# Kernel tuning notes

Measured on AMD Instinct MI355X. Metric: run time of the kernel, lower is better.

## Reference

```python
import jax, jax.numpy as jnp
import numpy as np

B, S, NH, D_IN = 64, 512, 4, 256   # batch, seq_len, rnn n_head, input_dim
H = 256                            # hidden_dim == attention activation_dim
AH = 256                           # attention_hidden_dim (attn out_dim)
OUT = 3                            # output_dim (sentiment classes)


def setup_inputs() -> dict:
    key = jax.random.key(0)
    ks = jax.random.split(key, 9)
    def p(k, shape, scale=0.05):
        return jax.random.normal(k, shape, dtype=jnp.float32) * scale
    return dict(
        x=jax.random.normal(ks[0], (B, S, NH, D_IN), dtype=jnp.float32),
        Wk=p(ks[1], (D_IN, H)), bk=jnp.zeros((H,), jnp.float32),
        Wq=p(ks[2], (H, H)),    bq=jnp.zeros((H,), jnp.float32),
        w_mlp=p(ks[3], (2 * H,)),
        Wproj=p(ks[4], (H, AH)), bproj=jnp.zeros((AH,), jnp.float32),
        W1=p(ks[5], (D_IN + AH, H)), b1=jnp.zeros((H,), jnp.float32),
        W2=p(ks[6], (H, H)),    b2=jnp.zeros((H,), jnp.float32),
        Wo=p(ks[7], (NH * H, OUT)), bo=jnp.zeros((OUT,), jnp.float32),
    )


def _cell(x_t, hidden, params):
    Wk, bk, Wq, bq, w_mlp, Wproj, bproj, W1, b1, W2, b2, Wo, bo = params
    kx = x_t @ Wk + bk           # [B, NH, H]  keys from step input
    qx = hidden @ Wq + bq        # [B, NH, H]  queries from hidden state
    w1, w2 = w_mlp[:H], w_mlp[H:]
    # MLP score: s[b,i,j] = tanh(cat(kx[b,j], qx[b,i]) . w) = tanh(kx[b,j].w1 + qx[b,i].w2)
    score = jnp.tanh((qx @ w2)[:, :, None] + (kx @ w1)[:, None, :])  # [B, NH, NH]
    score = jax.nn.softmax(score, axis=-1)
    attn = jnp.einsum('bij,bjh->bih', score, kx) @ Wproj + bproj     # [B, NH, AH]
    concat = jnp.concatenate([x_t, attn], axis=-1)                   # [B, NH, D_IN+AH]
    hidden_new = jax.nn.relu(concat @ W1 + b1) @ W2 + b2             # [B, NH, H]
    logits = hidden_new.reshape(B, NH * H) @ Wo + bo                 # [B, OUT]
    out = jax.nn.log_softmax(logits, axis=-1)
    return out, hidden_new


def reference(x, Wk, bk, Wq, bq, w_mlp, Wproj, bproj, W1, b1, W2, b2, Wo, bo):
    params = (Wk, bk, Wq, bq, w_mlp, Wproj, bproj, W1, b1, W2, b2, Wo, bo)
    h0 = jnp.zeros((B, NH, H), x.dtype)
    xs = jnp.swapaxes(x, 0, 1)  # [S, B, NH, D_IN] for scan over time
    def step(h, x_t):
        out, h_new = _cell(x_t, h, params)
        return h_new, out
    h_final, outs = jax.lax.scan(step, h0, xs)
    # return_sequence=False: last-step log-softmax output and final hidden
    return outs[-1], h_final
```

## Files before the change

kernel.cpp:

```cpp
#include <hip/hip_runtime.h>
#include <hip/hip_bf16.h>
#include <math.h>

#define BB   64
#define SS   512
#define NHH  4
#define DD   256
#define HH   256
#define LDH  264

typedef __attribute__((ext_vector_type(8))) short  short8;
typedef __attribute__((ext_vector_type(4))) float  floatx4;


__device__ __forceinline__ unsigned short f2b(float f) {
  __hip_bfloat16 h = __float2bfloat16(f);
  return __builtin_bit_cast(unsigned short, h);
}
__device__ __forceinline__ float b2f(unsigned short u) {
  unsigned v = (unsigned)u << 16;
  return __builtin_bit_cast(float, v);
}

__global__ __launch_bounds__(256) void init1_kernel(
    const float* __restrict__ Wk, const float* __restrict__ Wproj,
    const float* __restrict__ W1, const float* __restrict__ Wq,
    const float* __restrict__ bq, const float* __restrict__ w_mlp,
    const float* __restrict__ W2, const float* __restrict__ b2,
    const float* __restrict__ bk,
    float* __restrict__ ws, unsigned short* __restrict__ wpack)
{
  __shared__ float vsh[256];
  __shared__ float red[256];
  int tid = threadIdx.x;
  int b = blockIdx.x;

  if (b == 0) {
    const float* w2 = w_mlp + HH;
    {
      float a = 0.f;
      const float4* Wq4 = (const float4*)(Wq + tid * 256);
      const float4* w24 = (const float4*)w2;
      for (int k = 0; k < 64; ++k) {
        float4 wv = Wq4[k], xv = w24[k];
        a = fmaf(wv.x, xv.x, fmaf(wv.y, xv.y, fmaf(wv.z, xv.z, fmaf(wv.w, xv.w, a))));
      }
      vsh[tid] = a;
    }
    __syncthreads();
    {
      float a2 = 0.f;
      const float4* W24 = (const float4*)(W2 + tid * 256);
      const float4* v4  = (const float4*)vsh;
      for (int k = 0; k < 64; ++k) {
        float4 wv = W24[k], xv = v4[k];
        a2 = fmaf(wv.x, xv.x, fmaf(wv.y, xv.y, fmaf(wv.z, xv.z, fmaf(wv.w, xv.w, a2))));
      }
      ws[tid] = a2;
    }
    red[tid] = bq[tid] * w_mlp[HH + tid];
    __syncthreads();
    for (int s = 128; s; s >>= 1) { if (tid < s) red[tid] += red[tid + s]; __syncthreads(); }
    float c = red[0];
    __syncthreads();
    ws[768 + tid] = c;
    red[tid] = b2[tid] * vsh[tid];
    __syncthreads();
    for (int s = 128; s; s >>= 1) { if (tid < s) red[tid] += red[tid + s]; __syncthreads(); }
    if (tid == 0) ws[512] = red[0] + c;
    __syncthreads();
    red[tid] = bk[tid] * w_mlp[tid];
    __syncthreads();
    for (int s = 128; s; s >>= 1) { if (tid < s) red[tid] += red[tid + s]; __syncthreads(); }
    if (tid == 0) ws[513] = red[0];
    return;
  }

  if (b <= 256) {
    int idx = (b - 1) * 256 + tid;
    int j    = idx & 7;
    int lane = (idx >> 3) & 63;
    int ks   = (idx >> 9) & 7;
    int pan  = idx >> 12;
    int k = ks * 32 + ((lane >> 4) << 3) + j;
    int n = pan * 16 + (lane & 15);
    wpack[idx] = f2b(W1[k * 256 + n]);
    return;
  }

  {
    int r = b - 257;
    const float* w1b = W1 + 256 * 256;
    float acc = 0.f;
    for (int k = 0; k < 256; ++k)
      acc = fmaf(Wproj[r * 256 + k], w1b[k * 256 + tid], acc);
    ws[132096 + r * 256 + tid] = acc;
  }
}

__global__ __launch_bounds__(256) void init2_kernel(
    const float* __restrict__ Wk, const float* __restrict__ W1,
    const float* __restrict__ bproj, const float* __restrict__ bk,
    const float* __restrict__ w_mlp,
    float* __restrict__ ws, unsigned short* __restrict__ wpack)
{
  __shared__ float red[256];
  int tid = threadIdx.x;
  int b = blockIdx.x;
  const float* Wc = ws + 132096;

  if (b < 256) {
    int r = b;
    float acc = 0.f;
    for (int k = 0; k < 256; ++k)
      acc = fmaf(Wk[r * 256 + k], Wc[k * 256 + tid], acc);
    int n = tid;
    int pan = n >> 4, ks = r >> 5, j = r & 7;
    int lane = ((r >> 3) & 3) * 16 + (n & 15);
    wpack[65536 + pan * 4096 + ks * 512 + lane * 8 + j] = f2b(acc);
    red[tid] = Wk[r * 256 + tid] * w_mlp[tid];
    __syncthreads();
    for (int s = 128; s; s >>= 1) { if (tid < s) red[tid] += red[tid + s]; __syncthreads(); }
    if (tid == 0) ws[197632 + r] = red[0];
    return;
  }

  {
    const float* w1b = W1 + 256 * 256;
    float a3 = 0.f;
    for (int k = 0; k < 256; ++k)
      a3 = fmaf(bproj[k], w1b[k * 256 + tid], a3);
    for (int k = 0; k < 256; ++k)
      a3 = fmaf(bk[k], Wc[k * 256 + tid], a3);
    ws[256 + tid] = a3;
  }
}

__device__ __forceinline__ void mfma_gemm4(
    const unsigned short* A_lds, const short8* __restrict__ Bp,
    const float* __restrict__ bias, floatx4 acc[4][4], int l, int w)
{
  int col = l & 15, quad = l >> 4;
#pragma unroll
  for (int pp = 0; pp < 4; ++pp) {
    float bv = bias ? bias[(w * 4 + pp) * 16 + col] : 0.f;
#pragma unroll
    for (int mf = 0; mf < 4; ++mf)
      acc[mf][pp] = (floatx4){bv, bv, bv, bv};
  }
  const short8* Bb = Bp + (size_t)(w * 4) * 512 + l;
  short8 bb[3][4];
  short8 aa[2][4];
#pragma unroll
  for (int pp = 0; pp < 4; ++pp) bb[0][pp] = Bb[pp * 512];
#pragma unroll
  for (int pp = 0; pp < 4; ++pp) bb[1][pp] = Bb[pp * 512 + 64];
#pragma unroll
  for (int mf = 0; mf < 4; ++mf)
    aa[0][mf] = *(const short8*)(A_lds + (mf * 16 + col) * LDH + quad * 8);
#pragma unroll
  for (int kb = 0; kb < 8; ++kb) {
    if (kb + 2 < 8) {
#pragma unroll
      for (int pp = 0; pp < 4; ++pp)
        bb[(kb + 2) % 3][pp] = Bb[pp * 512 + (kb + 2) * 64];
    }
    if (kb + 1 < 8) {
#pragma unroll
      for (int mf = 0; mf < 4; ++mf)
        aa[(kb + 1) & 1][mf] =
            *(const short8*)(A_lds + (mf * 16 + col) * LDH + (kb + 1) * 32 + quad * 8);
    }
#pragma unroll
    for (int mf = 0; mf < 4; ++mf)
#pragma unroll
      for (int pp = 0; pp < 4; ++pp)
        acc[mf][pp] = __builtin_amdgcn_mfma_f32_16x16x32_bf16(
            aa[kb & 1][mf], bb[kb % 3][pp], acc[mf][pp], 0, 0, 0);
  }
}

__device__ __forceinline__ void acc_to_global(
    unsigned short* __restrict__ dst, const floatx4 acc[4][4],
    int l, int w, int b, int tt)
{
  int col = l & 15, quad = l >> 4;
#pragma unroll
  for (int mf = 0; mf < 4; ++mf)
#pragma unroll
    for (int r = 0; r < 4; ++r) {
      int m2 = mf * 16 + quad * 4 + r;
      size_t base = (((size_t)(tt * 16 + (m2 >> 2)) * 64 + b) * 4 + (m2 & 3)) * 256;
#pragma unroll
      for (int pp = 0; pp < 4; ++pp)
        dst[base + (w * 4 + pp) * 16 + col] = f2b(acc[mf][pp][r]);
    }
}

__device__ void precompute_block(
    int px, const float* __restrict__ x, const unsigned short* __restrict__ wpack,
    const float* __restrict__ b1, const float* __restrict__ ws,
    float* __restrict__ kw_c, unsigned short* __restrict__ xw1_c,
    unsigned short* __restrict__ kpw_c, int t0, char* smem)
{
  float* kwbuf = (float*)smem;
  unsigned short* XS = (unsigned short*)(smem + 2048);

  int b  = px & 63;
  int tt = px >> 6;
  int tid = threadIdx.x;
  int l = tid & 63, w = tid >> 6;

  const float4* xsrc = (const float4*)(x + (size_t)(b * SS + t0 + tt * 16) * NHH * DD);
#pragma unroll
  for (int i = 0; i < 16; ++i) {
    int f4 = i * 256 + tid;
    int r = f4 >> 6, c4 = f4 & 63;
    float4 v = xsrc[f4];
    ushort4 h;
    h.x = f2b(v.x); h.y = f2b(v.y); h.z = f2b(v.z); h.w = f2b(v.w);
    *(ushort4*)&XS[r * LDH + c4 * 4] = h;
  }
  __syncthreads();

  const short8* wpA = (const short8*)(wpack);
  const short8* wpD = (const short8*)(wpack + 65536);

  {
    const float* wkw = ws + 197632;
    float part = 0.f;
    const unsigned short* trow = XS + l * LDH + w * 64;
#pragma unroll
    for (int j8 = 0; j8 < 8; ++j8) {
      short8 tv = *(const short8*)(trow + j8 * 8);
#pragma unroll
      for (int j = 0; j < 8; ++j)
        part = fmaf(b2f((unsigned short)tv[j]), wkw[w * 64 + j8 * 8 + j], part);
    }
    kwbuf[l * 4 + w] = part;
  }

  floatx4 acc[4][4];

  mfma_gemm4(XS, wpA, b1, acc, l, w);
  acc_to_global(xw1_c, acc, l, w, b, tt);

  mfma_gemm4(XS, wpD, nullptr, acc, l, w);
  acc_to_global(kpw_c, acc, l, w, b, tt);

  __syncthreads();
  if (tid < 64) {
    float s = kwbuf[tid * 4] + kwbuf[tid * 4 + 1] + kwbuf[tid * 4 + 2] + kwbuf[tid * 4 + 3]
            + ws[513];
    kw_c[((size_t)(tt * 16 + (tid >> 2)) * 64 + b) * 4 + (tid & 3)] = s;
  }
}

__device__ __forceinline__ float wave_reduce_sum(float x) {
#define DPPSTEP(ctrl, rmask)                                                   \
  {                                                                            \
    int _s = __builtin_amdgcn_update_dpp(0, __builtin_bit_cast(int, x),        \
                                         (ctrl), (rmask), 0xf, true);          \
    x += __builtin_bit_cast(float, _s);                                        \
  }
  DPPSTEP(0x111, 0xf)
  DPPSTEP(0x112, 0xf)
  DPPSTEP(0x114, 0xf)
  DPPSTEP(0x118, 0xf)
  DPPSTEP(0x142, 0xa)
  DPPSTEP(0x143, 0xc)
#undef DPPSTEP
  return __builtin_bit_cast(float, __builtin_amdgcn_readlane(__builtin_bit_cast(int, x), 63));
}

__device__ __forceinline__ float tanh_fast(float y) {
  float ex = __expf(2.f * y);
  return 1.f - 2.f * __builtin_amdgcn_rcpf(ex + 1.f);
}

__device__ void seq_block(
    const unsigned short* __restrict__ xw1_c, const unsigned short* __restrict__ kpw_c,
    const float* __restrict__ kw_c, float* __restrict__ ws,
    float* __restrict__ relu_u, int t0, int n)
{
  int b = blockIdx.x;
  int tid = threadIdx.x;
  int i = tid >> 6, l = tid & 63;

  float4 v2v = ((const float4*)ws)[l];
  float4 cbv = ((const float4*)(ws + 256))[l];
  float c2 = ws[512];
  float qw = ws[768 + b * 4 + i];

  const ushort4* xw = (const ushort4*)xw1_c;
  const ushort4* kp = (const ushort4*)kpw_c;

  struct Slot { ushort4 x, k0, k1, k2, k3; float4 kw; };

  auto load = [&](Slot& s, int tc) {
    size_t rb_ = (size_t)(tc * 64 + b) * 4;
    s.x  = xw[(rb_ + i) * 64 + l];
    s.k0 = kp[(rb_ + 0) * 64 + l];
    s.k1 = kp[(rb_ + 1) * 64 + l];
    s.k2 = kp[(rb_ + 2) * 64 + l];
    s.k3 = kp[(rb_ + 3) * 64 + l];
    s.kw = *(const float4*)&kw_c[rb_];
  };

  auto step = [&](Slot& s, int t) {
    float e0 = tanh_fast(qw + s.kw.x);
    float e1 = tanh_fast(qw + s.kw.y);
    float e2 = tanh_fast(qw + s.kw.z);
    float e3 = tanh_fast(qw + s.kw.w);
    float q0 = __expf(e0), q1 = __expf(e1), q2 = __expf(e2), q3 = __expf(e3);
    float inv = __builtin_amdgcn_rcpf(q0 + q1 + q2 + q3);
    float4 K0 = {b2f(s.k0.x), b2f(s.k0.y), b2f(s.k0.z), b2f(s.k0.w)};
    float4 K1 = {b2f(s.k1.x), b2f(s.k1.y), b2f(s.k1.z), b2f(s.k1.w)};
    float4 K2 = {b2f(s.k2.x), b2f(s.k2.y), b2f(s.k2.z), b2f(s.k2.w)};
    float4 K3 = {b2f(s.k3.x), b2f(s.k3.y), b2f(s.k3.z), b2f(s.k3.w)};
    float4 X  = {b2f(s.x.x) + cbv.x, b2f(s.x.y) + cbv.y,
                 b2f(s.x.z) + cbv.z, b2f(s.x.w) + cbv.w};
    float4 a;
    a.x = fmaf(q0, K0.x, fmaf(q1, K1.x, fmaf(q2, K2.x, q3 * K3.x)));
    a.y = fmaf(q0, K0.y, fmaf(q1, K1.y, fmaf(q2, K2.y, q3 * K3.y)));
    a.z = fmaf(q0, K0.z, fmaf(q1, K1.z, fmaf(q2, K2.z, q3 * K3.z)));
    a.w = fmaf(q0, K0.w, fmaf(q1, K1.w, fmaf(q2, K2.w, q3 * K3.w)));
    float4 u;
    u.x = fmaf(a.x, inv, X.x); u.y = fmaf(a.y, inv, X.y);
    u.z = fmaf(a.z, inv, X.z); u.w = fmaf(a.w, inv, X.w);
    float4 r;
    r.x = fmaxf(u.x, 0.f); r.y = fmaxf(u.y, 0.f);
    r.z = fmaxf(u.z, 0.f); r.w = fmaxf(u.w, 0.f);
    float d = fmaf(r.x, v2v.x, fmaf(r.y, v2v.y, fmaf(r.z, v2v.z, r.w * v2v.w)));
    qw = wave_reduce_sum(d) + c2;
    if (t0 + t == SS - 1)
      *(float4*)&relu_u[(size_t)(b * 4 + i) * 256 + l * 4] = r;
  };

  Slot s0, s1, s2, s3;
  load(s0, 0); load(s1, 1); load(s2, 2); load(s3, 3);
  for (int t = 0; t < n; t += 4) {
    int nt;
    step(s0, t);     nt = t + 4; load(s0, nt < n ? nt : n - 1);
    step(s1, t + 1); nt = t + 5; load(s1, nt < n ? nt : n - 1);
    step(s2, t + 2); nt = t + 6; load(s2, nt < n ? nt : n - 1);
    step(s3, t + 3); nt = t + 7; load(s3, nt < n ? nt : n - 1);
  }
  if (l == 0) ws[768 + b * 4 + i] = qw;
}

__global__ __launch_bounds__(256, 2) void fused_kernel(
    const float* __restrict__ x, const unsigned short* __restrict__ wpack,
    const float* __restrict__ b1,
    float* kwB, unsigned short* xw1B, unsigned short* kpwB, int t0_pre,
    const float* kwA, const unsigned short* xw1A, const unsigned short* kpwA,
    int t0_seq, int n_seq,
    float* __restrict__ ws, float* __restrict__ relu_u)
{
  __shared__ __align__(16) char smem[2048 + 64 * LDH * 2];
  if (blockIdx.x < 64) {
    if (n_seq > 0) seq_block(xw1A, kpwA, kwA, ws, relu_u, t0_seq, n_seq);
    return;
  }
  precompute_block(blockIdx.x - 64, x, wpack, b1, ws,
                   kwB, xw1B, kpwB, t0_pre, smem);
}

__global__ __launch_bounds__(256) void final_hidden_kernel(
    const float* __restrict__ relu_u, const float* __restrict__ W2,
    const float* __restrict__ b2, float* __restrict__ out)
{
  __shared__ float rs[256];
  int row = blockIdx.x;
  int tid = threadIdx.x;
  rs[tid] = relu_u[(size_t)row * 256 + tid];
  __syncthreads();
  float acc = b2[tid];
  for (int k = 0; k < 256; ++k) acc = fmaf(rs[k], W2[k * 256 + tid], acc);
  out[192 + (size_t)row * 256 + tid] = acc;
}

__global__ __launch_bounds__(256) void final_logits_kernel(
    const float* __restrict__ hf, const float* __restrict__ Wo,
    const float* __restrict__ bo, float* __restrict__ outp)
{
  __shared__ float r0[256], r1[256], r2[256];
  int b = blockIdx.x;
  int tid = threadIdx.x;
  float a0 = 0.f, a1 = 0.f, a2 = 0.f;
  for (int k = tid; k < 1024; k += 256) {
    float h = hf[(size_t)b * 1024 + k];
    a0 = fmaf(h, Wo[k * 3 + 0], a0);
    a1 = fmaf(h, Wo[k * 3 + 1], a1);
    a2 = fmaf(h, Wo[k * 3 + 2], a2);
  }
  r0[tid] = a0; r1[tid] = a1; r2[tid] = a2;
  __syncthreads();
  for (int s = 128; s; s >>= 1) {
    if (tid < s) { r0[tid] += r0[tid + s]; r1[tid] += r1[tid + s]; r2[tid] += r2[tid + s]; }
    __syncthreads();
  }
  if (tid == 0) {
    float l0 = r0[0] + bo[0], l1 = r1[0] + bo[1], l2 = r2[0] + bo[2];
    float m = fmaxf(l0, fmaxf(l1, l2));
    float lse = m + logf(expf(l0 - m) + expf(l1 - m) + expf(l2 - m));
    outp[b * 3 + 0] = l0 - lse;
    outp[b * 3 + 1] = l1 - lse;
    outp[b * 3 + 2] = l2 - lse;
  }
}

extern "C" void kernel_launch(void* const* d_in, const int* in_sizes, int n_in,
                              void* d_out, int out_size, void* d_ws, size_t ws_size,
                              hipStream_t stream)
{
  const float* x     = (const float*)d_in[0];
  const float* Wk    = (const float*)d_in[1];
  const float* bk    = (const float*)d_in[2];
  const float* Wq    = (const float*)d_in[3];
  const float* bq    = (const float*)d_in[4];
  const float* w_mlp = (const float*)d_in[5];
  const float* Wproj = (const float*)d_in[6];
  const float* bproj = (const float*)d_in[7];
  const float* W1    = (const float*)d_in[8];
  const float* b1    = (const float*)d_in[9];
  const float* W2    = (const float*)d_in[10];
  const float* b2    = (const float*)d_in[11];
  const float* Wo    = (const float*)d_in[12];
  const float* bo    = (const float*)d_in[13];
  float* out = (float*)d_out;
  float* ws  = (float*)d_ws;

  float* ru = ws + 1024;
  unsigned short* wpack = (unsigned short*)(ws + 66560);
  const size_t OFF_CH = 197888;
  const long per_t = 256 + 65536;

  long ws_floats = (long)(ws_size / 4);
  long avail = ws_floats - (long)OFF_CH;

  int Tc = 128;
  while (Tc > 0 && 2L * Tc * per_t > avail) Tc -= 16;
  bool pipelined = (Tc >= 16);
  if (!pipelined) {
    Tc = 128;
    while (Tc > 16 && (long)Tc * per_t > avail) Tc -= 16;
  }

  float* bufA = ws + OFF_CH;
  float* bufB = pipelined ? bufA + (size_t)Tc * per_t : bufA;

  auto kw_of  = [&](float* base) { return base; };
  auto xw_of  = [&](float* base) { return (unsigned short*)(base + (size_t)Tc * 256); };
  auto kpw_of = [&](float* base) { return (unsigned short*)(base + (size_t)Tc * 256) + (size_t)Tc * 65536; };

  init1_kernel<<<513, 256, 0, stream>>>(Wk, Wproj, W1, Wq, bq, w_mlp, W2, b2, bk,
                                        ws, wpack);
  init2_kernel<<<257, 256, 0, stream>>>(Wk, W1, bproj, bk, w_mlp, ws, wpack);

  int C = (SS + Tc - 1) / Tc;

  if (pipelined) {
    for (int r = 0; r <= C; ++r) {
      bool hasPre = (r < C);
      bool hasSeq = (r >= 1);
      int t0p = r * Tc;
      int np  = hasPre ? ((SS - t0p) < Tc ? (SS - t0p) : Tc) : 0;
      int t0s = (r - 1) * Tc;
      int ns  = hasSeq ? ((SS - t0s) < Tc ? (SS - t0s) : Tc) : 0;
      float* pB = ((r & 1) ? bufB : bufA);
      float* pA = (((r - 1) & 1) ? bufB : bufA);
      int grid = 64 + (hasPre ? 64 * (np / 16) : 0);
      fused_kernel<<<grid, 256, 0, stream>>>(
          x, wpack, b1,
          kw_of(pB), xw_of(pB), kpw_of(pB), t0p,
          kw_of(pA), xw_of(pA), kpw_of(pA), t0s, ns,
          ws, ru);
    }
  } else {
    for (int c = 0; c < C; ++c) {
      int t0 = c * Tc;
      int n = (SS - t0) < Tc ? (SS - t0) : Tc;
      fused_kernel<<<64 + 64 * (n / 16), 256, 0, stream>>>(
          x, wpack, b1,
          kw_of(bufA), xw_of(bufA), kpw_of(bufA), t0,
          kw_of(bufA), xw_of(bufA), kpw_of(bufA), 0, 0,
          ws, ru);
      fused_kernel<<<64, 256, 0, stream>>>(
          x, wpack, b1,
          kw_of(bufA), xw_of(bufA), kpw_of(bufA), t0,
          kw_of(bufA), xw_of(bufA), kpw_of(bufA), t0, n,
          ws, ru);
    }
  }

  final_hidden_kernel<<<BB * NHH, 256, 0, stream>>>(ru, W2, b2, out);
  final_logits_kernel<<<BB, 256, 0, stream>>>(out + 192, Wo, bo, out);
}
```

Baseline: 436.6 us.

## Store precomputed chunks as fp32, fold bias and 2x scaling into init constants

Precomputed per-timestep projections (xw1 and kpw) are now stored in fp32 instead of bf16, so the serial recurrence no longer converts values and no longer adds a separate bias vector. The combined bias is folded into the GEMM bias in init. The tanh argument scaling by 2 is folded into the precomputed constants so each step computes tanh via one exp and one rcp. Launch bounds are relaxed to one block per SM and the prefetch is switched to pointer-increment refill. The cost is doubled workspace and memory traffic for the chunk buffers, which can shrink the chunk size, plus more register pressure.

```diff
diff --git a/kernel.cpp b/kernel.cpp
--- a/kernel.cpp
+++ b/kernel.cpp
@@ -56,23 +56,23 @@
         float4 wv = W24[k], xv = v4[k];
         a2 = fmaf(wv.x, xv.x, fmaf(wv.y, xv.y, fmaf(wv.z, xv.z, fmaf(wv.w, xv.w, a2))));
       }
-      ws[tid] = a2;
+      ws[tid] = 2.f * a2;
     }
     red[tid] = bq[tid] * w_mlp[HH + tid];
     __syncthreads();
     for (int s = 128; s; s >>= 1) { if (tid < s) red[tid] += red[tid + s]; __syncthreads(); }
     float c = red[0];
     __syncthreads();
-    ws[768 + tid] = c;
+    ws[768 + tid] = 2.f * c;
     red[tid] = b2[tid] * vsh[tid];
     __syncthreads();
     for (int s = 128; s; s >>= 1) { if (tid < s) red[tid] += red[tid + s]; __syncthreads(); }
-    if (tid == 0) ws[512] = red[0] + c;
+    if (tid == 0) ws[512] = 2.f * (red[0] + c);
     __syncthreads();
     red[tid] = bk[tid] * w_mlp[tid];
     __syncthreads();
     for (int s = 128; s; s >>= 1) { if (tid < s) red[tid] += red[tid + s]; __syncthreads(); }
-    if (tid == 0) ws[513] = red[0];
+    if (tid == 0) ws[513] = 2.f * red[0];
     return;
   }
 
@@ -101,7 +101,7 @@
 __global__ __launch_bounds__(256) void init2_kernel(
     const float* __restrict__ Wk, const float* __restrict__ W1,
     const float* __restrict__ bproj, const float* __restrict__ bk,
-    const float* __restrict__ w_mlp,
+    const float* __restrict__ w_mlp, const float* __restrict__ b1,
     float* __restrict__ ws, unsigned short* __restrict__ wpack)
 {
   __shared__ float red[256];
@@ -121,7 +121,7 @@
     red[tid] = Wk[r * 256 + tid] * w_mlp[tid];
     __syncthreads();
     for (int s = 128; s; s >>= 1) { if (tid < s) red[tid] += red[tid + s]; __syncthreads(); }
-    if (tid == 0) ws[197632 + r] = red[0];
+    if (tid == 0) ws[197632 + r] = 2.f * red[0];
     return;
   }
 
@@ -133,6 +133,7 @@
     for (int k = 0; k < 256; ++k)
       a3 = fmaf(bk[k], Wc[k * 256 + tid], a3);
     ws[256 + tid] = a3;
+    ws[197888 + tid] = a3 + b1[tid];
   }
 }
 
@@ -180,8 +181,8 @@
   }
 }
 
-__device__ __forceinline__ void acc_to_global(
-    unsigned short* __restrict__ dst, const floatx4 acc[4][4],
+__device__ __forceinline__ void acc_to_global_f32(
+    float* __restrict__ dst, const floatx4 acc[4][4],
     int l, int w, int b, int tt)
 {
   int col = l & 15, quad = l >> 4;
@@ -193,15 +194,15 @@
       size_t base = (((size_t)(tt * 16 + (m2 >> 2)) * 64 + b) * 4 + (m2 & 3)) * 256;
 #pragma unroll
       for (int pp = 0; pp < 4; ++pp)
-        dst[base + (w * 4 + pp) * 16 + col] = f2b(acc[mf][pp][r]);
+        dst[base + (w * 4 + pp) * 16 + col] = acc[mf][pp][r];
     }
 }
 
 __device__ void precompute_block(
     int px, const float* __restrict__ x, const unsigned short* __restrict__ wpack,
-    const float* __restrict__ b1, const float* __restrict__ ws,
-    float* __restrict__ kw_c, unsigned short* __restrict__ xw1_c,
-    unsigned short* __restrict__ kpw_c, int t0, char* smem)
+    const float* __restrict__ ws,
+    float* __restrict__ kw_c, float* __restrict__ xw1_c,
+    float* __restrict__ kpw_c, int t0, char* smem)
 {
   float* kwbuf = (float*)smem;
   unsigned short* XS = (unsigned short*)(smem + 2048);
@@ -242,11 +243,11 @@
 
   floatx4 acc[4][4];
 
-  mfma_gemm4(XS, wpA, b1, acc, l, w);
-  acc_to_global(xw1_c, acc, l, w, b, tt);
+  mfma_gemm4(XS, wpA, ws + 197888, acc, l, w);
+  acc_to_global_f32(xw1_c, acc, l, w, b, tt);
 
   mfma_gemm4(XS, wpD, nullptr, acc, l, w);
-  acc_to_global(kpw_c, acc, l, w, b, tt);
+  acc_to_global_f32(kpw_c, acc, l, w, b, tt);
 
   __syncthreads();
   if (tid < 64) {
@@ -273,13 +274,8 @@
   return __builtin_bit_cast(float, __builtin_amdgcn_readlane(__builtin_bit_cast(int, x), 63));
 }
 
-__device__ __forceinline__ float tanh_fast(float y) {
-  float ex = __expf(2.f * y);
-  return 1.f - 2.f * __builtin_amdgcn_rcpf(ex + 1.f);
-}
-
 __device__ void seq_block(
-    const unsigned short* __restrict__ xw1_c, const unsigned short* __restrict__ kpw_c,
+    const float* __restrict__ xw1_c, const float* __restrict__ kpw_c,
     const float* __restrict__ kw_c, float* __restrict__ ws,
     float* __restrict__ relu_u, int t0, int n)
 {
@@ -288,72 +284,73 @@
   int i = tid >> 6, l = tid & 63;
 
   float4 v2v = ((const float4*)ws)[l];
-  float4 cbv = ((const float4*)(ws + 256))[l];
-  float c2 = ws[512];
-  float qw = ws[768 + b * 4 + i];
-
-  const ushort4* xw = (const ushort4*)xw1_c;
-  const ushort4* kp = (const ushort4*)kpw_c;
-
-  struct Slot { ushort4 x, k0, k1, k2, k3; float4 kw; };
-
-  auto load = [&](Slot& s, int tc) {
-    size_t rb_ = (size_t)(tc * 64 + b) * 4;
-    s.x  = xw[(rb_ + i) * 64 + l];
-    s.k0 = kp[(rb_ + 0) * 64 + l];
-    s.k1 = kp[(rb_ + 1) * 64 + l];
-    s.k2 = kp[(rb_ + 2) * 64 + l];
-    s.k3 = kp[(rb_ + 3) * 64 + l];
-    s.kw = *(const float4*)&kw_c[rb_];
+  float c2s = ws[512];
+  float qw2 = ws[768 + b * 4 + i];
+
+  struct Slot { float4 x, k0, k1, k2, k3, kw; };
+  struct SP { const float4 *xp, *kp, *kw; };
+
+  const float4* xw4 = (const float4*)xw1_c;
+  const float4* kp4 = (const float4*)kpw_c;
+  const float4* kw4 = (const float4*)kw_c;
+
+  SP p0 = { xw4 + (b * 4 + i) * 64 + l,             kp4 + b * 256 + l,             kw4 + b };
+  SP p1 = { p0.xp + 16384, p0.kp + 16384, p0.kw + 64 };
+  SP p2 = { p1.xp + 16384, p1.kp + 16384, p1.kw + 64 };
+  SP p3 = { p2.xp + 16384, p2.kp + 16384, p2.kw + 64 };
+
+  auto refill = [&](Slot& s, SP& p) {
+    s.x  = *p.xp;
+    s.k0 = p.kp[0];
+    s.k1 = p.kp[64];
+    s.k2 = p.kp[128];
+    s.k3 = p.kp[192];
+    s.kw = *p.kw;
+    p.xp += 65536; p.kp += 65536; p.kw += 256;
   };
 
   auto step = [&](Slot& s, int t) {
-    float e0 = tanh_fast(qw + s.kw.x);
-    float e1 = tanh_fast(qw + s.kw.y);
-    float e2 = tanh_fast(qw + s.kw.z);
-    float e3 = tanh_fast(qw + s.kw.w);
-    float q0 = __expf(e0), q1 = __expf(e1), q2 = __expf(e2), q3 = __expf(e3);
-    float inv = __builtin_amdgcn_rcpf(q0 + q1 + q2 + q3);
-    float4 K0 = {b2f(s.k0.x), b2f(s.k0.y), b2f(s.k0.z), b2f(s.k0.w)};
-    float4 K1 = {b2f(s.k1.x), b2f(s.k1.y), b2f(s.k1.z), b2f(s.k1.w)};
-    float4 K2 = {b2f(s.k2.x), b2f(s.k2.y), b2f(s.k2.z), b2f(s.k2.w)};
-    float4 K3 = {b2f(s.k3.x), b2f(s.k3.y), b2f(s.k3.z), b2f(s.k3.w)};
-    float4 X  = {b2f(s.x.x) + cbv.x, b2f(s.x.y) + cbv.y,
-                 b2f(s.x.z) + cbv.z, b2f(s.x.w) + cbv.w};
+    float r0 = __builtin_amdgcn_rcpf(__expf(qw2 + s.kw.x) + 1.f);
+    float r1 = __builtin_amdgcn_rcpf(__expf(qw2 + s.kw.y) + 1.f);
+    float r2 = __builtin_amdgcn_rcpf(__expf(qw2 + s.kw.z) + 1.f);
+    float r3 = __builtin_amdgcn_rcpf(__expf(qw2 + s.kw.w) + 1.f);
+    float q0 = __expf(fmaf(-2.f, r0, 1.f));
+    float q1 = __expf(fmaf(-2.f, r1, 1.f));
+    float q2 = __expf(fmaf(-2.f, r2, 1.f));
+    float q3 = __expf(fmaf(-2.f, r3, 1.f));
+    float inv = __builtin_amdgcn_rcpf((q0 + q1) + (q2 + q3));
     float4 a;
-    a.x = fmaf(q0, K0.x, fmaf(q1, K1.x, fmaf(q2, K2.x, q3 * K3.x)));
-    a.y = fmaf(q0, K0.y, fmaf(q1, K1.y, fmaf(q2, K2.y, q3 * K3.y)));
-    a.z = fmaf(q0, K0.z, fmaf(q1, K1.z, fmaf(q2, K2.z, q3 * K3.z)));
-    a.w = fmaf(q0, K0.w, fmaf(q1, K1.w, fmaf(q2, K2.w, q3 * K3.w)));
+    a.x = fmaf(q0, s.k0.x, fmaf(q1, s.k1.x, fmaf(q2, s.k2.x, q3 * s.k3.x)));
+    a.y = fmaf(q0, s.k0.y, fmaf(q1, s.k1.y, fmaf(q2, s.k2.y, q3 * s.k3.y)));
+    a.z = fmaf(q0, s.k0.z, fmaf(q1, s.k1.z, fmaf(q2, s.k2.z, q3 * s.k3.z)));
+    a.w = fmaf(q0, s.k0.w, fmaf(q1, s.k1.w, fmaf(q2, s.k2.w, q3 * s.k3.w)));
     float4 u;
-    u.x = fmaf(a.x, inv, X.x); u.y = fmaf(a.y, inv, X.y);
-    u.z = fmaf(a.z, inv, X.z); u.w = fmaf(a.w, inv, X.w);
-    float4 r;
-    r.x = fmaxf(u.x, 0.f); r.y = fmaxf(u.y, 0.f);
-    r.z = fmaxf(u.z, 0.f); r.w = fmaxf(u.w, 0.f);
-    float d = fmaf(r.x, v2v.x, fmaf(r.y, v2v.y, fmaf(r.z, v2v.z, r.w * v2v.w)));
-    qw = wave_reduce_sum(d) + c2;
+    u.x = fmaf(a.x, inv, s.x.x); u.y = fmaf(a.y, inv, s.x.y);
+    u.z = fmaf(a.z, inv, s.x.z); u.w = fmaf(a.w, inv, s.x.w);
+    float4 rr;
+    rr.x = fmaxf(u.x, 0.f); rr.y = fmaxf(u.y, 0.f);
+    rr.z = fmaxf(u.z, 0.f); rr.w = fmaxf(u.w, 0.f);
+    float d = fmaf(rr.x, v2v.x, rr.y * v2v.y) + fmaf(rr.z, v2v.z, rr.w * v2v.w);
+    qw2 = wave_reduce_sum(d) + c2s;
     if (t0 + t == SS - 1)
-      *(float4*)&relu_u[(size_t)(b * 4 + i) * 256 + l * 4] = r;
+      *(float4*)&relu_u[(size_t)(b * 4 + i) * 256 + l * 4] = rr;
   };
 
   Slot s0, s1, s2, s3;
-  load(s0, 0); load(s1, 1); load(s2, 2); load(s3, 3);
+  refill(s0, p0); refill(s1, p1); refill(s2, p2); refill(s3, p3);
   for (int t = 0; t < n; t += 4) {
-    int nt;
-    step(s0, t);     nt = t + 4; load(s0, nt < n ? nt : n - 1);
-    step(s1, t + 1); nt = t + 5; load(s1, nt < n ? nt : n - 1);
-    step(s2, t + 2); nt = t + 6; load(s2, nt < n ? nt : n - 1);
-    step(s3, t + 3); nt = t + 7; load(s3, nt < n ? nt : n - 1);
-  }
-  if (l == 0) ws[768 + b * 4 + i] = qw;
-}
-
-__global__ __launch_bounds__(256, 2) void fused_kernel(
+    step(s0, t);     refill(s0, p0);
+    step(s1, t + 1); refill(s1, p1);
+    step(s2, t + 2); refill(s2, p2);
+    step(s3, t + 3); refill(s3, p3);
+  }
+  if (l == 0) ws[768 + b * 4 + i] = qw2;
+}
+
+__global__ __launch_bounds__(256, 1) void fused_kernel(
     const float* __restrict__ x, const unsigned short* __restrict__ wpack,
-    const float* __restrict__ b1,
-    float* kwB, unsigned short* xw1B, unsigned short* kpwB, int t0_pre,
-    const float* kwA, const unsigned short* xw1A, const unsigned short* kpwA,
+    float* kwB, float* xw1B, float* kpwB, int t0_pre,
+    const float* kwA, const float* xw1A, const float* kpwA,
     int t0_seq, int n_seq,
     float* __restrict__ ws, float* __restrict__ relu_u)
 {
@@ -362,7 +359,7 @@
     if (n_seq > 0) seq_block(xw1A, kpwA, kwA, ws, relu_u, t0_seq, n_seq);
     return;
   }
-  precompute_block(blockIdx.x - 64, x, wpack, b1, ws,
+  precompute_block(blockIdx.x - 64, x, wpack, ws,
                    kwB, xw1B, kpwB, t0_pre, smem);
 }
 
@@ -433,11 +430,11 @@
 
   float* ru = ws + 1024;
   unsigned short* wpack = (unsigned short*)(ws + 66560);
-  const size_t OFF_CH = 197888;
-  const long per_t = 256 + 65536;
+  const size_t OFF_CH = 198144;
+  const long per_t = 256 + 2 * 65536;
 
   long ws_floats = (long)(ws_size / 4);
-  long avail = ws_floats - (long)OFF_CH;
+  long avail = ws_floats - (long)OFF_CH - 8L * per_t;
 
   int Tc = 128;
   while (Tc > 0 && 2L * Tc * per_t > avail) Tc -= 16;
@@ -451,12 +448,12 @@
   float* bufB = pipelined ? bufA + (size_t)Tc * per_t : bufA;
 
   auto kw_of  = [&](float* base) { return base; };
-  auto xw_of  = [&](float* base) { return (unsigned short*)(base + (size_t)Tc * 256); };
-  auto kpw_of = [&](float* base) { return (unsigned short*)(base + (size_t)Tc * 256) + (size_t)Tc * 65536; };
+  auto xw_of  = [&](float* base) { return base + (size_t)Tc * 256; };
+  auto kpw_of = [&](float* base) { return base + (size_t)Tc * 256 + (size_t)Tc * 65536; };
 
   init1_kernel<<<513, 256, 0, stream>>>(Wk, Wproj, W1, Wq, bq, w_mlp, W2, b2, bk,
                                         ws, wpack);
-  init2_kernel<<<257, 256, 0, stream>>>(Wk, W1, bproj, bk, w_mlp, ws, wpack);
+  init2_kernel<<<257, 256, 0, stream>>>(Wk, W1, bproj, bk, w_mlp, b1, ws, wpack);
 
   int C = (SS + Tc - 1) / Tc;
 
@@ -472,7 +469,7 @@
       float* pA = (((r - 1) & 1) ? bufB : bufA);
       int grid = 64 + (hasPre ? 64 * (np / 16) : 0);
       fused_kernel<<<grid, 256, 0, stream>>>(
-          x, wpack, b1,
+          x, wpack,
           kw_of(pB), xw_of(pB), kpw_of(pB), t0p,
           kw_of(pA), xw_of(pA), kpw_of(pA), t0s, ns,
           ws, ru);
@@ -482,12 +479,12 @@
       int t0 = c * Tc;
       int n = (SS - t0) < Tc ? (SS - t0) : Tc;
       fused_kernel<<<64 + 64 * (n / 16), 256, 0, stream>>>(
-          x, wpack, b1,
+          x, wpack,
           kw_of(bufA), xw_of(bufA), kpw_of(bufA), t0,
           kw_of(bufA), xw_of(bufA), kpw_of(bufA), 0, 0,
           ws, ru);
       fused_kernel<<<64, 256, 0, stream>>>(
-          x, wpack, b1,
+          x, wpack,
           kw_of(bufA), xw_of(bufA), kpw_of(bufA), t0,
           kw_of(bufA), xw_of(bufA), kpw_of(bufA), t0, n,
           ws, ru);
```

After: 412.1 us. -5.6%, faster.
